# Kernel optimization log

Hardware: AMD Instinct MI355X
Metric: run time of the kernel (lower is better)

Reference implementation:

```python
import jax, jax.numpy as jnp
import numpy as np

K = 1024  # codebook size
D = 256   # embedding dim


def setup_inputs() -> dict:
    key = jax.random.key(0)
    k1, k2 = jax.random.split(key)
    z_e_x = jax.random.normal(k1, (32, D, 32, 32), dtype=jnp.float32)  # NCHW
    # nn.Embedding weight initialized uniform(-1/K, 1/K)
    W = jax.random.uniform(k2, (K, D), dtype=jnp.float32, minval=-1.0 / K, maxval=1.0 / K)
    return {"z_e_x": z_e_x, "W": W}


def reference(z_e_x, W):
    # permute NCHW -> NHWC, flatten spatial, nearest-codebook lookup (vq)
    z = jnp.transpose(z_e_x, (0, 2, 3, 1))            # [B, H, Wd, D]
    B, H, Wd, Dd = z.shape
    flat = z.reshape(-1, Dd)                           # [N, D]
    # squared L2 distances: ||z||^2 - 2 z.W^T + ||W||^2
    z_sq = jnp.sum(flat * flat, axis=1, keepdims=True)         # [N, 1]
    w_sq = jnp.sum(W * W, axis=1)                               # [K]
    dists = z_sq - 2.0 * (flat @ W.T) + w_sq[None, :]           # [N, K]
    idx = jnp.argmin(dists, axis=1)                             # [N]
    latents = idx.reshape(B, H, Wd)                             # [B, H, Wd] int indices
    return latents
```

## Files before the change

kernel.cpp:

```cpp
#include <hip/hip_runtime.h>

#define NPOS 32768
#define DDIM 256
#define KCODES 1024

typedef __attribute__((ext_vector_type(8))) short bf16x8;
typedef __attribute__((ext_vector_type(4))) float f32x4;
typedef unsigned long long u64;

__device__ __forceinline__ float sqr_rn(float x) {
    float r = x * x;
    asm volatile("" : "+v"(r));
    return r;
}
__device__ __forceinline__ float add_rn(float a, float b) {
    float r = a + b;
    asm volatile("" : "+v"(r));
    return r;
}

__device__ __forceinline__ unsigned short f2bf(float x) {
    unsigned u = __float_as_uint(x);
    return (unsigned short)((u + 0x7fffu + ((u >> 16) & 1u)) >> 16);
}

__device__ __forceinline__ u64 packm(float s, int code) {
    unsigned b = __float_as_uint(s);
    unsigned mm = ((unsigned)((int)b >> 31)) | 0x80000000u;
    return ((u64)(b ^ mm) << 32) | (unsigned)code;
}

__global__ __launch_bounds__(256) void prep(const float* __restrict__ z,
                                            const float* __restrict__ W,
                                            float* __restrict__ wsq,
                                            unsigned short* __restrict__ zb16t,
                                            unsigned short* __restrict__ wb16t) {
    __shared__ unsigned short Ls[8 * 1024];
    const int t = threadIdx.x;
    if (blockIdx.x < 1024) {
        const int img = blockIdx.x >> 5;
        const int dc  = blockIdx.x & 31;
        const int kk  = dc >> 2, kq = dc & 3;
        const float* zr = z + img * (DDIM * 1024) + dc * 8 * 1024;
#pragma unroll
        for (int e = 0; e < 8; ++e) {
            const float4 v = *(const float4*)&zr[e * 1024 + t * 4];
            unsigned short* o = &Ls[e * 1024 + t * 4];
            o[0] = f2bf(v.x); o[1] = f2bf(v.y); o[2] = f2bf(v.z); o[3] = f2bf(v.w);
        }
        __syncthreads();
#pragma unroll
        for (int j = 0; j < 4; ++j) {
            const int m = t + j * 256;
            const int mtile = img * 8 + (m >> 7);
            bf16x8 o;
#pragma unroll
            for (int e = 0; e < 8; ++e) o[e] = (short)Ls[e * 1024 + m];
            *(bf16x8*)&zb16t[mtile * 32768 + kk * 4096 + kq * 1024 + (m & 127) * 8] = o;
        }
    } else {
        const int bid = blockIdx.x - 1024;
        const int row = bid * 16 + (t >> 4);
        const int j   = t & 15;
        const float* base = W + row * DDIM + (j & 7) + (j >> 3) * 128;
        float r = sqr_rn(base[0]);
#pragma unroll
        for (int i = 1; i < 16; ++i) r = add_rn(r, sqr_rn(base[i * 8]));
#pragma unroll
        for (int m = 1; m <= 8; m <<= 1) r = add_rn(r, __shfl_xor(r, m));
        if (j == 0) wsq[row] = r;
#pragma unroll
        for (int jj = 0; jj < 2; ++jj) {
            const int u  = t + jj * 256;
            const int n  = bid * 16 + (u >> 5);
            const int k8 = u & 31;
            const float4 f0 = *(const float4*)&W[n * DDIM + k8 * 8];
            const float4 f1 = *(const float4*)&W[n * DDIM + k8 * 8 + 4];
            bf16x8 o;
            o[0] = (short)f2bf(f0.x); o[1] = (short)f2bf(f0.y);
            o[2] = (short)f2bf(f0.z); o[3] = (short)f2bf(f0.w);
            o[4] = (short)f2bf(f1.x); o[5] = (short)f2bf(f1.y);
            o[6] = (short)f2bf(f1.z); o[7] = (short)f2bf(f1.w);
            const int kk = k8 >> 2, kq = k8 & 3;
            *(bf16x8*)&wb16t[(n >> 8) * 65536 + kk * 8192 + kq * 2048 + (n & 255) * 8] = o;
        }
    }
}

__global__ __launch_bounds__(256) __attribute__((amdgpu_waves_per_eu(2, 2)))
void gemm_top2(const unsigned short* __restrict__ zb16t,
               const unsigned short* __restrict__ wb16t,
               const float* __restrict__ wsq, u64* __restrict__ cand) {
    __shared__ u64 redU[4096];

    const int t    = threadIdx.x;
    const int w    = t >> 6;
    const int l    = t & 63;
    const int ln   = l & 15;
    const int q    = l >> 4;
    const int mw   = (w & 1) * 64;
    const int nw   = (w >> 1) * 128;
    const int mblk = blockIdx.x >> 2;
    const int nblk = blockIdx.x & 3;
    const int m0   = mblk * 128;
    const int n0   = nblk * 256;

    const char* aLane = (const char*)zb16t + (size_t)mblk * 65536 + q * 2048 + (mw + ln) * 16;
    const char* bLane = (const char*)wb16t + (size_t)nblk * 131072 + q * 4096 + (nw + ln) * 16;

    f32x4 acc[4][8];
#pragma unroll
    for (int a = 0; a < 4; ++a)
#pragma unroll
        for (int b = 0; b < 8; ++b) acc[a][b] = (f32x4)(0.f);

#pragma unroll 1
    for (int kk = 0; kk < 8; ++kk) {
        bf16x8 afr[4], bfr[8];
#pragma unroll
        for (int mf = 0; mf < 4; ++mf)
            afr[mf] = *(const bf16x8*)(aLane + kk * 8192 + mf * 256);
#pragma unroll
        for (int nf = 0; nf < 8; ++nf)
            bfr[nf] = *(const bf16x8*)(bLane + kk * 16384 + nf * 256);
#pragma unroll
        for (int nf = 0; nf < 8; ++nf)
#pragma unroll
            for (int mf = 0; mf < 4; ++mf)
                acc[mf][nf] = __builtin_amdgcn_mfma_f32_16x16x32_bf16(
                    afr[mf], bfr[nf], acc[mf][nf], 0, 0, 0);
    }

    float wq[8];
#pragma unroll
    for (int nf = 0; nf < 8; ++nf) wq[nf] = wsq[n0 + nw + nf * 16 + ln];

#pragma unroll
    for (int mf = 0; mf < 4; ++mf) {
#pragma unroll
        for (int reg = 0; reg < 4; ++reg) {
            const int row = mw + mf * 16 + q * 4 + reg;
            float s0 = 1e30f, s1 = 1e30f;
            int   i0 = 0,     i1 = 0;
#pragma unroll
            for (int nf = 0; nf < 8; ++nf) {
                const float s  = fmaf(-2.f, acc[mf][nf][reg], wq[nf]);
                const int   cc = n0 + nw + nf * 16 + ln;
                if (s < s0)      { s1 = s0; i1 = i0; s0 = s; i0 = cc; }
                else if (s < s1) { s1 = s; i1 = cc; }
            }
            u64 p0 = packm(s0, i0), p1 = packm(s1, i1);
            const u64 o0 = __shfl_xor(p0, 1);
            const u64 o1 = __shfl_xor(p1, 1);
            const u64 c0 = (p0 < o0) ? p0 : o0;
            const u64 hi = (p0 < o0) ? o0 : p0;
            const u64 lo = (p1 < o1) ? p1 : o1;
            const u64 c1 = (hi < lo) ? hi : lo;
            if ((ln & 1) == 0) {
                u64* slot = &redU[row * 32 + (w >> 1) * 16 + (ln >> 1) * 2];
                slot[0] = c0;
                slot[1] = c1;
            }
        }
    }
    __syncthreads();
    {
        const int r2 = t >> 1, half = t & 1;
        u64 c0 = ~0ull, c1 = ~0ull;
#pragma unroll
        for (int j = 0; j < 16; ++j) {
            const u64 v = redU[r2 * 32 + half * 16 + j];
            if (v < c0)      { c1 = c0; c0 = v; }
            else if (v < c1) { c1 = v; }
        }
        __syncthreads();
        redU[r2 * 4 + half * 2]     = c0;
        redU[r2 * 4 + half * 2 + 1] = c1;
    }
    __syncthreads();
    if (t < 128) {
        const u64 a = redU[t * 4], b = redU[t * 4 + 1];
        const u64 c = redU[t * 4 + 2], d = redU[t * 4 + 3];
        const u64 m1 = (a < c) ? a : c;
        const u64 hi = (a < c) ? c : a;
        const u64 lo = (b < d) ? b : d;
        const u64 m2 = (hi < lo) ? hi : lo;
        u64* o = &cand[(u64)(m0 + t) * 8 + nblk * 2];
        o[0] = m1;
        o[1] = m2;
    }
}

#define ZS 260
__global__ __launch_bounds__(256) void rescore(const float* __restrict__ z,
                                               const float* __restrict__ W,
                                               const float* __restrict__ wsq,
                                               const u64* __restrict__ cand,
                                               int* __restrict__ out) {
    __shared__ float Zs[32 * ZS];
    const int t  = threadIdx.x;
    const int m0 = blockIdx.x * 32;
    const float* zimg = z + (m0 >> 10) * (DDIM * 1024) + (m0 & 1023);
#pragma unroll
    for (int j = 0; j < 8; ++j) {
        const int f4 = t + j * 256;
        const int d = f4 >> 3, p4 = f4 & 7;
        const float4 v = *(const float4*)&zimg[d * 1024 + p4 * 4];
        Zs[(p4 * 4 + 0) * ZS + d] = v.x;
        Zs[(p4 * 4 + 1) * ZS + d] = v.y;
        Zs[(p4 * 4 + 2) * ZS + d] = v.z;
        Zs[(p4 * 4 + 3) * ZS + d] = v.w;
    }
    __syncthreads();
    const int pl = t >> 3, slot = t & 7;
    const int p = m0 + pl;
    const float* zr = &Zs[pl * ZS];

    float h0 = sqr_rn(zr[slot]);
    float h1 = sqr_rn(zr[128 + slot]);
#pragma unroll
    for (int i = 1; i < 16; ++i) {
        h0 = add_rn(h0, sqr_rn(zr[slot + 8 * i]));
        h1 = add_rn(h1, sqr_rn(zr[128 + slot + 8 * i]));
    }
#pragma unroll
    for (int m = 1; m <= 4; m <<= 1) {
        h0 = add_rn(h0, __shfl_xor(h0, m));
        h1 = add_rn(h1, __shfl_xor(h1, m));
    }
    const float zq = add_rn(h0, h1);

    const int code = (int)(unsigned)(cand[(u64)p * 8 + slot] & 0xffffffffULL);
    const float* wr = W + code * DDIM;
    float M = 0.f;
#pragma unroll 8
    for (int d4 = 0; d4 < 64; ++d4) {
        const float4 zv = *(const float4*)&zr[d4 * 4];
        const float4 wv = *(const float4*)&wr[d4 * 4];
        M = fmaf(zv.x, wv.x, M);
        M = fmaf(zv.y, wv.y, M);
        M = fmaf(zv.z, wv.z, M);
        M = fmaf(zv.w, wv.w, M);
    }
    const float s = add_rn(fmaf(-2.f, M, zq), wsq[code]);
    u64 v = ((u64)__float_as_uint(s) << 32) | (unsigned)code;
#pragma unroll
    for (int m = 1; m <= 4; m <<= 1) {
        const u64 o = __shfl_xor(v, m);
        if (o < v) v = o;
    }
    if (slot == 0) out[p] = (int)(unsigned)(v & 0xffffffffULL);
}

extern "C" void kernel_launch(void* const* d_in, const int* in_sizes, int n_in,
                              void* d_out, int out_size, void* d_ws, size_t ws_size,
                              hipStream_t stream) {
    const float* z = (const float*)d_in[0];
    const float* W = (const float*)d_in[1];
    int* out = (int*)d_out;

    char* ws = (char*)d_ws;
    float*          wsq   = (float*)ws;
    u64*            cand  = (u64*)(ws + 4096);
    unsigned short* zb16t = (unsigned short*)(ws + 2101248);
    unsigned short* wb16t = (unsigned short*)(ws + 18878464);

    prep<<<1024 + KCODES / 16, 256, 0, stream>>>(z, W, wsq, zb16t, wb16t);
    gemm_top2<<<(NPOS / 128) * 4, 256, 0, stream>>>(zb16t, wb16t, wsq, cand);
    rescore<<<NPOS / 32, 256, 0, stream>>>(z, W, wsq, cand, out);
}
```

Baseline: 153.3 us.

## Halve GEMM N-tile, double-buffer fragment loads, widen rescore candidates to 16

```diff
diff --git a/kernel.cpp b/kernel.cpp
--- a/kernel.cpp
+++ b/kernel.cpp
@@ -82,58 +82,77 @@
             o[4] = (short)f2bf(f1.x); o[5] = (short)f2bf(f1.y);
             o[6] = (short)f2bf(f1.z); o[7] = (short)f2bf(f1.w);
             const int kk = k8 >> 2, kq = k8 & 3;
-            *(bf16x8*)&wb16t[(n >> 8) * 65536 + kk * 8192 + kq * 2048 + (n & 255) * 8] = o;
-        }
-    }
-}
-
-__global__ __launch_bounds__(256) __attribute__((amdgpu_waves_per_eu(2, 2)))
+            *(bf16x8*)&wb16t[(n >> 7) * 32768 + kk * 4096 + kq * 1024 + (n & 127) * 8] = o;
+        }
+    }
+}
+
+__global__ __launch_bounds__(256) __attribute__((amdgpu_waves_per_eu(3, 4)))
 void gemm_top2(const unsigned short* __restrict__ zb16t,
                const unsigned short* __restrict__ wb16t,
                const float* __restrict__ wsq, u64* __restrict__ cand) {
-    __shared__ u64 redU[4096];
-
-    const int t    = threadIdx.x;
-    const int w    = t >> 6;
-    const int l    = t & 63;
-    const int ln   = l & 15;
-    const int q    = l >> 4;
-    const int mw   = (w & 1) * 64;
-    const int nw   = (w >> 1) * 128;
-    const int mblk = blockIdx.x >> 2;
-    const int nblk = blockIdx.x & 3;
-    const int m0   = mblk * 128;
-    const int n0   = nblk * 256;
+    __shared__ u64 redL[512];
+
+    const int t     = threadIdx.x;
+    const int w     = t >> 6;
+    const int l     = t & 63;
+    const int ln    = l & 15;
+    const int q     = l >> 4;
+    const int mw    = (w & 1) * 64;
+    const int nw    = (w >> 1) * 64;
+    const int mblk  = blockIdx.x >> 3;
+    const int ntile = blockIdx.x & 7;
+    const int m0    = mblk * 128;
+    const int n0    = ntile * 128;
 
     const char* aLane = (const char*)zb16t + (size_t)mblk * 65536 + q * 2048 + (mw + ln) * 16;
-    const char* bLane = (const char*)wb16t + (size_t)nblk * 131072 + q * 4096 + (nw + ln) * 16;
-
-    f32x4 acc[4][8];
+    const char* bLane = (const char*)wb16t + (size_t)ntile * 65536 + q * 2048 + (nw + ln) * 16;
+
+    f32x4 acc[4][4];
 #pragma unroll
     for (int a = 0; a < 4; ++a)
 #pragma unroll
-        for (int b = 0; b < 8; ++b) acc[a][b] = (f32x4)(0.f);
+        for (int b = 0; b < 4; ++b) acc[a][b] = (f32x4)(0.f);
+
+    bf16x8 a0[4], b0[4], a1[4], b1[4];
+#pragma unroll
+    for (int f = 0; f < 4; ++f) {
+        a0[f] = *(const bf16x8*)(aLane + f * 256);
+        b0[f] = *(const bf16x8*)(bLane + f * 256);
+    }
 
 #pragma unroll 1
-    for (int kk = 0; kk < 8; ++kk) {
-        bf16x8 afr[4], bfr[8];
-#pragma unroll
-        for (int mf = 0; mf < 4; ++mf)
-            afr[mf] = *(const bf16x8*)(aLane + kk * 8192 + mf * 256);
-#pragma unroll
-        for (int nf = 0; nf < 8; ++nf)
-            bfr[nf] = *(const bf16x8*)(bLane + kk * 16384 + nf * 256);
-#pragma unroll
-        for (int nf = 0; nf < 8; ++nf)
+    for (int kp = 0; kp < 4; ++kp) {
+        const int ke = kp * 2;
+#pragma unroll
+        for (int f = 0; f < 4; ++f) {
+            a1[f] = *(const bf16x8*)(aLane + (ke + 1) * 8192 + f * 256);
+            b1[f] = *(const bf16x8*)(bLane + (ke + 1) * 8192 + f * 256);
+        }
+#pragma unroll
+        for (int nf = 0; nf < 4; ++nf)
 #pragma unroll
             for (int mf = 0; mf < 4; ++mf)
                 acc[mf][nf] = __builtin_amdgcn_mfma_f32_16x16x32_bf16(
-                    afr[mf], bfr[nf], acc[mf][nf], 0, 0, 0);
-    }
-
-    float wq[8];
-#pragma unroll
-    for (int nf = 0; nf < 8; ++nf) wq[nf] = wsq[n0 + nw + nf * 16 + ln];
+                    a0[mf], b0[nf], acc[mf][nf], 0, 0, 0);
+        if (kp < 3) {
+#pragma unroll
+            for (int f = 0; f < 4; ++f) {
+                a0[f] = *(const bf16x8*)(aLane + (ke + 2) * 8192 + f * 256);
+                b0[f] = *(const bf16x8*)(bLane + (ke + 2) * 8192 + f * 256);
+            }
+        }
+#pragma unroll
+        for (int nf = 0; nf < 4; ++nf)
+#pragma unroll
+            for (int mf = 0; mf < 4; ++mf)
+                acc[mf][nf] = __builtin_amdgcn_mfma_f32_16x16x32_bf16(
+                    a1[mf], b1[nf], acc[mf][nf], 0, 0, 0);
+    }
+
+    float wq[4];
+#pragma unroll
+    for (int nf = 0; nf < 4; ++nf) wq[nf] = wsq[n0 + nw + nf * 16 + ln];
 
 #pragma unroll
     for (int mf = 0; mf < 4; ++mf) {
@@ -143,56 +162,45 @@
             float s0 = 1e30f, s1 = 1e30f;
             int   i0 = 0,     i1 = 0;
 #pragma unroll
-            for (int nf = 0; nf < 8; ++nf) {
+            for (int nf = 0; nf < 4; ++nf) {
                 const float s  = fmaf(-2.f, acc[mf][nf][reg], wq[nf]);
                 const int   cc = n0 + nw + nf * 16 + ln;
                 if (s < s0)      { s1 = s0; i1 = i0; s0 = s; i0 = cc; }
                 else if (s < s1) { s1 = s; i1 = cc; }
             }
             u64 p0 = packm(s0, i0), p1 = packm(s1, i1);
-            const u64 o0 = __shfl_xor(p0, 1);
-            const u64 o1 = __shfl_xor(p1, 1);
-            const u64 c0 = (p0 < o0) ? p0 : o0;
-            const u64 hi = (p0 < o0) ? o0 : p0;
-            const u64 lo = (p1 < o1) ? p1 : o1;
-            const u64 c1 = (hi < lo) ? hi : lo;
-            if ((ln & 1) == 0) {
-                u64* slot = &redU[row * 32 + (w >> 1) * 16 + (ln >> 1) * 2];
-                slot[0] = c0;
-                slot[1] = c1;
-            }
-        }
-    }
-    __syncthreads();
-    {
-        const int r2 = t >> 1, half = t & 1;
-        u64 c0 = ~0ull, c1 = ~0ull;
-#pragma unroll
-        for (int j = 0; j < 16; ++j) {
-            const u64 v = redU[r2 * 32 + half * 16 + j];
-            if (v < c0)      { c1 = c0; c0 = v; }
-            else if (v < c1) { c1 = v; }
-        }
-        __syncthreads();
-        redU[r2 * 4 + half * 2]     = c0;
-        redU[r2 * 4 + half * 2 + 1] = c1;
+#pragma unroll
+            for (int m = 1; m <= 8; m <<= 1) {
+                const u64 o0 = __shfl_xor(p0, m);
+                const u64 o1 = __shfl_xor(p1, m);
+                const u64 c0 = (p0 < o0) ? p0 : o0;
+                const u64 hi = (p0 < o0) ? o0 : p0;
+                const u64 lo = (p1 < o1) ? p1 : o1;
+                p0 = c0;
+                p1 = (hi < lo) ? hi : lo;
+            }
+            if (ln == 0) {
+                redL[row * 4 + (w >> 1) * 2]     = p0;
+                redL[row * 4 + (w >> 1) * 2 + 1] = p1;
+            }
+        }
     }
     __syncthreads();
     if (t < 128) {
-        const u64 a = redU[t * 4], b = redU[t * 4 + 1];
-        const u64 c = redU[t * 4 + 2], d = redU[t * 4 + 3];
+        const u64 a = redL[t * 4], b = redL[t * 4 + 1];
+        const u64 c = redL[t * 4 + 2], d = redL[t * 4 + 3];
         const u64 m1 = (a < c) ? a : c;
         const u64 hi = (a < c) ? c : a;
         const u64 lo = (b < d) ? b : d;
         const u64 m2 = (hi < lo) ? hi : lo;
-        u64* o = &cand[(u64)(m0 + t) * 8 + nblk * 2];
+        u64* o = &cand[(u64)(m0 + t) * 16 + ntile * 2];
         o[0] = m1;
         o[1] = m2;
     }
 }
 
 #define ZS 260
-__global__ __launch_bounds__(256) void rescore(const float* __restrict__ z,
+__global__ __launch_bounds__(512) void rescore(const float* __restrict__ z,
                                                const float* __restrict__ W,
                                                const float* __restrict__ wsq,
                                                const u64* __restrict__ cand,
@@ -202,8 +210,8 @@
     const int m0 = blockIdx.x * 32;
     const float* zimg = z + (m0 >> 10) * (DDIM * 1024) + (m0 & 1023);
 #pragma unroll
-    for (int j = 0; j < 8; ++j) {
-        const int f4 = t + j * 256;
+    for (int j = 0; j < 4; ++j) {
+        const int f4 = t + j * 512;
         const int d = f4 >> 3, p4 = f4 & 7;
         const float4 v = *(const float4*)&zimg[d * 1024 + p4 * 4];
         Zs[(p4 * 4 + 0) * ZS + d] = v.x;
@@ -212,25 +220,20 @@
         Zs[(p4 * 4 + 3) * ZS + d] = v.w;
     }
     __syncthreads();
-    const int pl = t >> 3, slot = t & 7;
+    const int pl = t >> 4, slot = t & 15;
     const int p = m0 + pl;
     const float* zr = &Zs[pl * ZS];
 
-    float h0 = sqr_rn(zr[slot]);
-    float h1 = sqr_rn(zr[128 + slot]);
-#pragma unroll
-    for (int i = 1; i < 16; ++i) {
-        h0 = add_rn(h0, sqr_rn(zr[slot + 8 * i]));
-        h1 = add_rn(h1, sqr_rn(zr[128 + slot + 8 * i]));
-    }
-#pragma unroll
-    for (int m = 1; m <= 4; m <<= 1) {
-        h0 = add_rn(h0, __shfl_xor(h0, m));
-        h1 = add_rn(h1, __shfl_xor(h1, m));
-    }
-    const float zq = add_rn(h0, h1);
-
-    const int code = (int)(unsigned)(cand[(u64)p * 8 + slot] & 0xffffffffULL);
+    const int sl8 = slot & 7;
+    const int hb  = (slot >> 3) * 128;
+    float h = sqr_rn(zr[hb + sl8]);
+#pragma unroll
+    for (int i = 1; i < 16; ++i) h = add_rn(h, sqr_rn(zr[hb + sl8 + 8 * i]));
+#pragma unroll
+    for (int m = 1; m <= 4; m <<= 1) h = add_rn(h, __shfl_xor(h, m));
+    const float zq = add_rn(h, __shfl_xor(h, 8));
+
+    const int code = (int)(unsigned)(cand[(u64)p * 16 + slot] & 0xffffffffULL);
     const float* wr = W + code * DDIM;
     float M = 0.f;
 #pragma unroll 8
@@ -245,7 +248,7 @@
     const float s = add_rn(fmaf(-2.f, M, zq), wsq[code]);
     u64 v = ((u64)__float_as_uint(s) << 32) | (unsigned)code;
 #pragma unroll
-    for (int m = 1; m <= 4; m <<= 1) {
+    for (int m = 1; m <= 8; m <<= 1) {
         const u64 o = __shfl_xor(v, m);
         if (o < v) v = o;
     }
@@ -262,10 +265,10 @@
     char* ws = (char*)d_ws;
     float*          wsq   = (float*)ws;
     u64*            cand  = (u64*)(ws + 4096);
-    unsigned short* zb16t = (unsigned short*)(ws + 2101248);
-    unsigned short* wb16t = (unsigned short*)(ws + 18878464);
+    unsigned short* zb16t = (unsigned short*)(ws + 4198400);
+    unsigned short* wb16t = (unsigned short*)(ws + 20975616);
 
     prep<<<1024 + KCODES / 16, 256, 0, stream>>>(z, W, wsq, zb16t, wb16t);
-    gemm_top2<<<(NPOS / 128) * 4, 256, 0, stream>>>(zb16t, wb16t, wsq, cand);
-    rescore<<<NPOS / 32, 256, 0, stream>>>(z, W, wsq, cand, out);
-}
+    gemm_top2<<<(NPOS / 128) * 8, 256, 0, stream>>>(zb16t, wb16t, wsq, cand);
+    rescore<<<NPOS / 32, 512, 0, stream>>>(z, W, wsq, cand, out);
+}
```

New measurement: 182.1 us. 18.8% more time.
